# Optimization experiments

Measured on AMD Instinct MI355X. Metric: run time of the kernel, lower is better.

Reference implementation:

```python
import jax, jax.numpy as jnp
import numpy as np

MEAN, STD = 0.1307, 0.3081  # standard MNIST Normalization layer
FC = [784, 2048, 2048, 2048, 2048, 10]


def _forward_boxes(W, b, low, high):
    # swap bounds where weights are negative (interval arithmetic)
    Wn = jnp.where(W < 0, W, 0.0)
    Wp = jnp.where(W >= 0, W, 0.0)
    low_out = high @ Wn.T + low @ Wp.T + b
    high_out = low @ Wn.T + high @ Wp.T + b
    return low_out, high_out


def _abstract_relu(x, low, high):
    # vectorized DeepPoly relaxation (original loops per neuron)
    crossing = (low < 0) & (high > 0)
    denom = jnp.where(crossing, high - low, 1.0)  # safe denom
    ub_slope = jnp.where(crossing, high / denom, 0.0)
    ub_int = jnp.where(crossing, -(low * high) / denom, 0.0)
    lam = jnp.where(low * low > high * high, 0.0, 1.0)  # minimum-area lambda
    keep = jnp.where(high <= 0.0, 0.0, 1.0)  # identity diag unless dead neuron
    w_high = jnp.where(crossing, ub_slope, keep)
    w_low = jnp.where(crossing, lam, keep)
    b_high = ub_int
    x_out = jnp.maximum(x, 0.0)
    return x_out, w_low * low, w_high * high + b_high, (w_low, w_high, b_high)


def _back_sub_relu(M, w_high, w_low, b_high, is_high):
    # vectorized version of the original double python loop; w_* are the
    # relu diagonals ([in]), M is the accumulated backsub matrix [out,in]
    mask = (w_high != 0.0).astype(M.dtype)
    if is_high:
        out = jnp.where(M > 0, M * w_high, M * w_low) * mask
        bias = (jnp.maximum(M, 0.0) * mask) @ b_high
    else:
        out = jnp.where(M > 0, M * w_low, M * w_high) * mask
        bias = (jnp.minimum(M, 0.0) * mask) @ b_high
    return out, bias


def _back_sub(records, low0, high0, out_size):
    dt = low0.dtype
    Wl = jnp.eye(out_size, dtype=dt)
    Wh = jnp.eye(out_size, dtype=dt)
    bl = jnp.zeros(out_size, dtype=dt)
    bh = jnp.zeros(out_size, dtype=dt)
    for kind, data in reversed(records):
        if kind == 'linear':
            W, b = data
            bh = bh + Wh @ b
            bl = bl + Wl @ b
            Wh = Wh @ W
            Wl = Wl @ W
        else:  # relu
            wl, wh, bhr = data
            Wh, dbh = _back_sub_relu(Wh, wh, wl, bhr, True)
            Wl, dbl = _back_sub_relu(Wl, wh, wl, bhr, False)
            bh = bh + dbh
            bl = bl + dbl
    low_out, _ = _forward_boxes(Wl, bl, low0, high0)
    _, high_out = _forward_boxes(Wh, bh, low0, high0)
    return low_out, high_out


def _forward(x, low, high, params):
    norm = lambda t: ((t - MEAN) / STD).reshape(-1)
    x, low, high = norm(x), norm(low), norm(high)
    low0, high0 = low, high
    records = []
    n = len(params)
    for i, (W, b) in enumerate(params):
        x = W @ x + b
        records.append(('linear', (W, b)))
        # box bounds from forward_boxes are immediately replaced by backsub
        low, high = _back_sub(records, low0, high0, W.shape[0])
        if i + 1 < n:
            x, low, high, rdata = _abstract_relu(x, low, high)
            records.append(('relu', rdata))
    return x, low, high


def setup_inputs() -> dict:
    key = jax.random.key(0)
    ks = jax.random.split(key, 11)
    x = jax.random.normal(ks[0], (1, 1, 28, 28), dtype=jnp.float32)
    eps = 0.05
    inp = {"x": x, "low": x - eps, "high": x + eps}
    for i in range(5):
        fi, fo = FC[i], FC[i + 1]
        inp[f"W{i+1}"] = jax.random.normal(ks[1 + 2 * i], (fo, fi), dtype=jnp.float32) * float(1.0 / np.sqrt(fi))
        inp[f"b{i+1}"] = jax.random.normal(ks[2 + 2 * i], (fo,), dtype=jnp.float32) * 0.01
    return inp


def reference(x, low, high, W1, b1, W2, b2, W3, b3, W4, b4, W5, b5):
    params = [(W1, b1), (W2, b2), (W3, b3), (W4, b4), (W5, b5)]
    return _forward(x, low, high, params)
```

## Files before the change

### kernel.cpp

```cpp
#include <hip/hip_runtime.h>
#include <hip/hip_bf16.h>


#define MEAN_C 0.1307f
#define STD_C  0.3081f

#define OFF_X0     0u
#define OFF_X1     2048u
#define OFF_L0     4096u
#define OFF_H0     5120u
#define OFF_WL     6144u
#define OFF_WH     14336u
#define OFF_BHR    22528u
#define OFF_BOXA   30720u
#define OFF_BOXB   34816u
#define OFF_BIASA  38912u
#define OFF_BIASB  43008u
#define OFF_B20    47104u
#define OFF_W0TH   47136u
#define OFF_W0TL   964640u
#define OFF_W1TH   1882144u
#define OFF_W1TL   3979296u
#define OFF_W2TH   6076448u
#define OFF_W2TL   8173600u
#define OFF_AH0    10270752u
#define OFF_AL0    14465056u
#define OFF_AH1    18659360u
#define OFF_AL1    22853664u
#define OFF_PPA    18659360u
#define OFF_PPB    18987040u
#define OFF_PPC    19314720u
#define OFF_PPD    19642400u

typedef _Float16 half8 __attribute__((ext_vector_type(8)));
typedef float floatx4 __attribute__((ext_vector_type(4)));

__device__ __forceinline__ void gl2lds16(const void* g, void* l) {
    __builtin_amdgcn_global_load_lds(
        (const __attribute__((address_space(1))) unsigned int*)g,
        (__attribute__((address_space(3))) unsigned int*)l, 16, 0, 0);
}

__device__ __forceinline__ float blockReduce256(float v) {
    #pragma unroll
    for (int o = 32; o > 0; o >>= 1) v += __shfl_down(v, o, 64);
    __shared__ float sred[4];
    int w = threadIdx.x >> 6;
    if ((threadIdx.x & 63) == 0) sred[w] = v;
    __syncthreads();
    float r = 0.f;
    if (threadIdx.x == 0) r = sred[0] + sred[1] + sred[2] + sred[3];
    return r;
}

__device__ __forceinline__ float2 blockReduce256x2(float a, float b) {
    #pragma unroll
    for (int o = 32; o > 0; o >>= 1) {
        a += __shfl_down(a, o, 64);
        b += __shfl_down(b, o, 64);
    }
    __shared__ float sa[4], sb[4];
    int w = threadIdx.x >> 6;
    if ((threadIdx.x & 63) == 0) { sa[w] = a; sb[w] = b; }
    __syncthreads();
    float2 r = {0.f, 0.f};
    if (threadIdx.x == 0) {
        r.x = sa[0] + sa[1] + sa[2] + sa[3];
        r.y = sb[0] + sb[1] + sb[2] + sb[3];
    }
    return r;
}

__device__ __forceinline__ void relu_rec_calc(float h, float l,
                                              float& vwl, float& vwh, float& vbh) {
    if (h <= 0.f)      { vwl = 0.f; vwh = 0.f; vbh = 0.f; }
    else if (l >= 0.f) { vwl = 1.f; vwh = 1.f; vbh = 0.f; }
    else {
        float d = h - l;
        vwh = h / d;
        vbh = -(l * h) / d;
        vwl = (l * l > h * h) ? 0.f : 1.f;
    }
}

__global__ void k_norm(const float* __restrict__ x, const float* __restrict__ lo,
                       const float* __restrict__ hi, float* __restrict__ ws) {
    int i = blockIdx.x * blockDim.x + threadIdx.x;
    if (i < 784) {
        ws[OFF_X0 + i] = (x[i]  - MEAN_C) / STD_C;
        ws[OFF_L0 + i] = (lo[i] - MEAN_C) / STD_C;
        ws[OFF_H0 + i] = (hi[i] - MEAN_C) / STD_C;
    } else if (i < 896) {
        ws[OFF_L0 + i] = 0.f;
        ws[OFF_H0 + i] = 0.f;
    }
}

__global__ void k_fboxes0(const float* __restrict__ W0, const float* __restrict__ b0,
                          const float* __restrict__ x0,
                          const float* __restrict__ lo0, const float* __restrict__ hi0,
                          float* __restrict__ box, float* __restrict__ xout) {
    int r = blockIdx.x;
    int srow = r & 2047;
    int is_high = r < 2048;
    const float* Wr = W0 + (size_t)srow * 784;
    float acc = 0.f, accx = 0.f;
    for (int c = threadIdx.x; c < 784; c += 256) {
        float m = Wr[c];
        if (is_high) acc += (m < 0.f) ? m * lo0[c] : m * hi0[c];
        else         acc += (m < 0.f) ? m * hi0[c] : m * lo0[c];
        accx += m * x0[c];
    }
    float2 rr = blockReduce256x2(acc, accx);
    if (threadIdx.x == 0) {
        box[r] = rr.x + b0[srow];
        if (is_high) xout[r] = rr.y + b0[r];
    }
}

__global__ __launch_bounds__(256) void k_relu_split(
        const float* __restrict__ Wi, const float* __restrict__ xin,
        const float* __restrict__ boxPrev, const float* __restrict__ biasPrev,
        float* __restrict__ recWL, float* __restrict__ recWH, float* __restrict__ recBH,
        const float* __restrict__ bj, const float* __restrict__ bvi,
        float* __restrict__ bias, float* __restrict__ boxOut,
        float* __restrict__ xout,
        _Float16* __restrict__ Ahi, _Float16* __restrict__ Alo) {
    int row = blockIdx.x;
    int is_high = row < 2048;
    int srow = row & 2047;
    const float* src = Wi + (size_t)srow * 2048;
    int c0 = threadIdx.x * 8;
    float mv[8], bxh[8], bxl[8], abj[8], ax[8];
    *(float4*)&mv[0]  = *(const float4*)(src + c0);
    *(float4*)&mv[4]  = *(const float4*)(src + c0 + 4);
    *(float4*)&bxh[0] = *(const float4*)(boxPrev + c0);
    *(float4*)&bxh[4] = *(const float4*)(boxPrev + c0 + 4);
    *(float4*)&bxl[0] = *(const float4*)(boxPrev + 2048 + c0);
    *(float4*)&bxl[4] = *(const float4*)(boxPrev + 2048 + c0 + 4);
    *(float4*)&abj[0] = *(const float4*)(bj + c0);
    *(float4*)&abj[4] = *(const float4*)(bj + c0 + 4);
    *(float4*)&ax[0]  = *(const float4*)(xin + c0);
    *(float4*)&ax[4]  = *(const float4*)(xin + c0 + 4);
    if (biasPrev) {
        float ph[8], pl[8];
        *(float4*)&ph[0] = *(const float4*)(biasPrev + c0);
        *(float4*)&ph[4] = *(const float4*)(biasPrev + c0 + 4);
        *(float4*)&pl[0] = *(const float4*)(biasPrev + 2048 + c0);
        *(float4*)&pl[4] = *(const float4*)(biasPrev + 2048 + c0 + 4);
        #pragma unroll
        for (int e = 0; e < 8; e++) { bxh[e] += ph[e]; bxl[e] += pl[e]; }
    }
    float acc = 0.f, accx = 0.f;
    float rl[8], rh[8], rb[8];
    half8 hi, lo;
    #pragma unroll
    for (int e = 0; e < 8; e++) {
        relu_rec_calc(bxh[e], bxl[e], rl[e], rh[e], rb[e]);
        float m = mv[e];
        float t, bt;
        if (is_high) { t = (m > 0.f) ? m * rh[e] : m * rl[e]; bt = fmaxf(m, 0.f) * rb[e]; }
        else         { t = (m > 0.f) ? m * rl[e] : m * rh[e]; bt = fminf(m, 0.f) * rb[e]; }
        acc += bt + t * abj[e];
        accx += m * fmaxf(ax[e], 0.f);
        _Float16 h = (_Float16)t;
        hi[e] = h;
        lo[e] = (_Float16)(t - (float)h);
    }
    *(half8*)(Ahi + (size_t)row * 2048 + c0) = hi;
    *(half8*)(Alo + (size_t)row * 2048 + c0) = lo;
    if (row == 0) {
        *(float4*)(recWL + c0) = *(float4*)&rl[0];
        *(float4*)(recWL + c0 + 4) = *(float4*)&rl[4];
        *(float4*)(recWH + c0) = *(float4*)&rh[0];
        *(float4*)(recWH + c0 + 4) = *(float4*)&rh[4];
        *(float4*)(recBH + c0) = *(float4*)&rb[0];
        *(float4*)(recBH + c0 + 4) = *(float4*)&rb[4];
    }
    float2 rr = blockReduce256x2(acc, accx);
    if (threadIdx.x == 0) {
        bias[row] = bvi[srow] + rr.x;
        boxOut[row] = 0.f;
        if (is_high) xout[row] = rr.y + bvi[row];
    }
}

__global__ void k_transpose_split(const float* __restrict__ W, int NC,
                                  _Float16* __restrict__ Thi,
                                  _Float16* __restrict__ Tlo) {
    __shared__ float s[32][33];
    int c = threadIdx.x & 31;
    int r = threadIdx.x >> 5;
    #pragma unroll
    for (int rr = 0; rr < 4; rr++) {
        int k = blockIdx.y * 32 + r + rr * 8;
        int n = blockIdx.x * 32 + c;
        float v = (n < NC) ? W[(size_t)k * NC + n] : 0.f;
        s[c][r + rr * 8] = v;
    }
    __syncthreads();
    #pragma unroll
    for (int rr = 0; rr < 4; rr++) {
        int nl = r + rr * 8;
        float v = s[nl][c];
        _Float16 h = (_Float16)v;
        size_t o = (size_t)(blockIdx.x * 32 + nl) * 2048 + blockIdx.y * 32 + c;
        Thi[o] = h;
        Tlo[o] = (_Float16)(v - (float)h);
    }
}

template<int NT, int EPI>
__global__ __launch_bounds__(256, 2) void k_gemm(
        const _Float16* __restrict__ Ah, const _Float16* __restrict__ Al,
        const _Float16* __restrict__ Bh, const _Float16* __restrict__ Bl,
        const float* __restrict__ wl, const float* __restrict__ wh,
        const float* __restrict__ bhr, const float* __restrict__ bj,
        float* __restrict__ bias,
        _Float16* __restrict__ oAh, _Float16* __restrict__ oAl,
        const float* __restrict__ lo0, const float* __restrict__ hi0,
        float* __restrict__ box) {
    __shared__ _Float16 sAh[128 * 32], sAl[128 * 32];
    __shared__ _Float16 sBh[NT * 32 * 32], sBl[NT * 32 * 32];
    int tid = threadIdx.x;
    int row0 = blockIdx.y * 128, col0 = blockIdx.x * (NT * 32);

    int cr = tid >> 2;
    int q  = (tid & 3) ^ (cr & 3);
    const _Float16* gAh0 = Ah + (size_t)(row0 + cr) * 2048 + q * 8;
    const _Float16* gAh1 = gAh0 + (size_t)64 * 2048;
    const _Float16* gAl0 = Al + (size_t)(row0 + cr) * 2048 + q * 8;
    const _Float16* gAl1 = gAl0 + (size_t)64 * 2048;
    const _Float16* gBh0 = Bh + (size_t)(col0 + cr) * 2048 + q * 8;
    const _Float16* gBl0 = Bl + (size_t)(col0 + cr) * 2048 + q * 8;
    const _Float16* gBh1 = gBh0 + (size_t)64 * 2048;
    const _Float16* gBl1 = gBl0 + (size_t)64 * 2048;
    _Float16* lAh0 = &sAh[tid * 8];
    _Float16* lAh1 = &sAh[tid * 8 + 2048];
    _Float16* lAl0 = &sAl[tid * 8];
    _Float16* lAl1 = &sAl[tid * 8 + 2048];
    _Float16* lBh0 = &sBh[tid * 8];
    _Float16* lBl0 = &sBl[tid * 8];
    _Float16* lBh1 = &sBh[tid * 8 + 2048];
    _Float16* lBl1 = &sBl[tid * 8 + 2048];

    int lane = tid & 63, wv = tid >> 6;
    int wm = wv & 1, wn = wv >> 1;
    int l15 = lane & 15, lq = lane >> 4;
    int soff = (lq ^ (l15 & 3)) * 8;
    int arow = wm * 64 + l15;
    int brow = wn * (NT * 16) + l15;

    floatx4 acc[4][NT];
    floatx4 z = {0.f, 0.f, 0.f, 0.f};
    #pragma unroll
    for (int i = 0; i < 4; i++)
        #pragma unroll
        for (int j = 0; j < NT; j++) acc[i][j] = z;

    for (int k0 = 0; k0 < 2048; k0 += 32) {
        gl2lds16(gAh0 + k0, lAh0);
        gl2lds16(gAh1 + k0, lAh1);
        gl2lds16(gAl0 + k0, lAl0);
        gl2lds16(gAl1 + k0, lAl1);
        gl2lds16(gBh0 + k0, lBh0);
        gl2lds16(gBl0 + k0, lBl0);
        if (NT == 4) {
            gl2lds16(gBh1 + k0, lBh1);
            gl2lds16(gBl1 + k0, lBl1);
        }
        __syncthreads();
        half8 bh[NT], bl[NT];
        #pragma unroll
        for (int nt = 0; nt < NT; nt++) {
            bh[nt] = *(const half8*)&sBh[(brow + nt * 16) * 32 + soff];
            bl[nt] = *(const half8*)&sBl[(brow + nt * 16) * 32 + soff];
        }
        #pragma unroll
        for (int mt = 0; mt < 4; mt++) {
            half8 ah = *(const half8*)&sAh[(arow + mt * 16) * 32 + soff];
            half8 al = *(const half8*)&sAl[(arow + mt * 16) * 32 + soff];
            #pragma unroll
            for (int nt = 0; nt < NT; nt++) {
                acc[mt][nt] = __builtin_amdgcn_mfma_f32_16x16x32_f16(ah, bh[nt], acc[mt][nt], 0, 0, 0);
                acc[mt][nt] = __builtin_amdgcn_mfma_f32_16x16x32_f16(al, bh[nt], acc[mt][nt], 0, 0, 0);
                acc[mt][nt] = __builtin_amdgcn_mfma_f32_16x16x32_f16(ah, bl[nt], acc[mt][nt], 0, 0, 0);
            }
        }
        __syncthreads();
    }

    int is_high = row0 < 2048;
    float bsum[4][4];
    #pragma unroll
    for (int mt = 0; mt < 4; mt++)
        #pragma unroll
        for (int r = 0; r < 4; r++) bsum[mt][r] = 0.f;

    #pragma unroll
    for (int nt = 0; nt < NT; nt++) {
        int gc = col0 + wn * (NT * 16) + nt * 16 + l15;
        if (EPI == 0) {
            float cwl = wl[gc], cwh = wh[gc], cbh = bhr[gc], cbj = bj[gc];
            #pragma unroll
            for (int mt = 0; mt < 4; mt++) {
                #pragma unroll
                for (int r = 0; r < 4; r++) {
                    float m = acc[mt][nt][r];
                    float t, bt;
                    if (is_high) { t = (m > 0.f) ? m * cwh : m * cwl; bt = fmaxf(m, 0.f) * cbh; }
                    else         { t = (m > 0.f) ? m * cwl : m * cwh; bt = fminf(m, 0.f) * cbh; }
                    bsum[mt][r] += bt + t * cbj;
                    int grow = row0 + wm * 64 + mt * 16 + lq * 4 + r;
                    size_t o = (size_t)grow * 2048 + gc;
                    _Float16 h = (_Float16)t;
                    oAh[o] = h;
                    oAl[o] = (_Float16)(t - (float)h);
                }
            }
        } else {
            float clo = lo0[gc], chi = hi0[gc];
            #pragma unroll
            for (int mt = 0; mt < 4; mt++) {
                #pragma unroll
                for (int r = 0; r < 4; r++) {
                    float m = acc[mt][nt][r];
                    float contrib;
                    if (is_high) contrib = (m < 0.f) ? m * clo : m * chi;
                    else         contrib = (m < 0.f) ? m * chi : m * clo;
                    bsum[mt][r] += contrib;
                }
            }
        }
    }
    #pragma unroll
    for (int mt = 0; mt < 4; mt++) {
        #pragma unroll
        for (int r = 0; r < 4; r++) {
            float v = bsum[mt][r];
            v += __shfl_xor(v, 1);
            v += __shfl_xor(v, 2);
            v += __shfl_xor(v, 4);
            v += __shfl_xor(v, 8);
            if (l15 == 0) {
                int grow = row0 + wm * 64 + mt * 16 + lq * 4 + r;
                if (EPI == 0) atomicAdd(&bias[grow], v);
                else          atomicAdd(&box[grow], v);
            }
        }
    }
}

__global__ void k_relu_rec(const float* __restrict__ box, const float* __restrict__ bias,
                           float* __restrict__ wl, float* __restrict__ wh,
                           float* __restrict__ bhr) {
    int i = blockIdx.x * blockDim.x + threadIdx.x;
    float h = box[i] + bias[i];
    float l = box[2048 + i] + bias[2048 + i];
    float vwl, vwh, vbh;
    relu_rec_calc(h, l, vwl, vwh, vbh);
    wl[i] = vwl; wh[i] = vwh; bhr[i] = vbh;
}

__global__ __launch_bounds__(256) void k_skinny2(
        const float* __restrict__ src, int bcast,
        const float* __restrict__ wl, const float* __restrict__ wh,
        const float* __restrict__ W, int N, float* __restrict__ Ppart) {
    __shared__ float sA[20 * 256];
    __shared__ float sRed[20 * 128];
    int ky = blockIdx.y, k0 = ky * 256;
    int tid = threadIdx.x;
    for (int idx = tid; idx < 20 * 256; idx += 256) {
        int r = idx >> 8, c = idx & 255;
        int gc = k0 + c;
        float m;
        if (bcast) m = src[(size_t)(r % 10) * 2048 + gc];
        else {
            m = 0.f;
            #pragma unroll
            for (int p = 0; p < 8; p++)
                m += src[(size_t)p * 40960 + (size_t)r * 2048 + gc];
        }
        float t = (r < 10) ? ((m > 0.f) ? m * wh[gc] : m * wl[gc])
                           : ((m > 0.f) ? m * wl[gc] : m * wh[gc]);
        sA[idx] = t;
    }
    __syncthreads();
    int c = blockIdx.x * 128 + (tid & 127);
    int kh = tid >> 7;
    float acc[20];
    #pragma unroll
    for (int r = 0; r < 20; r++) acc[r] = 0.f;
    if (c < N) {
        const float* Wp = W + (size_t)(k0 + kh * 128) * N + c;
        for (int kk = 0; kk < 128; kk++) {
            float w = Wp[(size_t)kk * N];
            #pragma unroll
            for (int r = 0; r < 20; r++) acc[r] += sA[r * 256 + kh * 128 + kk] * w;
        }
    }
    if (kh == 1 && c < N) {
        #pragma unroll
        for (int r = 0; r < 20; r++) sRed[r * 128 + (tid & 127)] = acc[r];
    }
    __syncthreads();
    if (kh == 0 && c < N) {
        #pragma unroll
        for (int r = 0; r < 20; r++)
            Ppart[(size_t)ky * 40960 + (size_t)r * 2048 + c] =
                acc[r] + sRed[r * 128 + (tid & 127)];
    }
}

__global__ void k_bias20(const float* __restrict__ W4,
                         const float* __restrict__ PPa, const float* __restrict__ PPb,
                         const float* __restrict__ PPc,
                         const float* __restrict__ WLr, const float* __restrict__ WHr,
                         const float* __restrict__ BHr,
                         const float* __restrict__ b0, const float* __restrict__ b1,
                         const float* __restrict__ b2, const float* __restrict__ b3,
                         const float* __restrict__ b4,
                         const float* __restrict__ x3,
                         float* __restrict__ bias20, float* __restrict__ out) {
    int row = blockIdx.x;
    int is_high = row < 10;
    int srow = row % 10;
    float acc = 0.f, accx = 0.f;
    for (int c = threadIdx.x; c < 2048; c += 256) {
        {
            float m = W4[(size_t)srow * 2048 + c];
            float wlv = WLr[3 * 2048 + c], whv = WHr[3 * 2048 + c], bhv = BHr[3 * 2048 + c];
            float t  = is_high ? ((m > 0.f) ? m * whv : m * wlv) : ((m > 0.f) ? m * wlv : m * whv);
            float bt = is_high ? fmaxf(m, 0.f) * bhv : fminf(m, 0.f) * bhv;
            acc += bt + t * b3[c];
            accx += m * fmaxf(x3[c], 0.f);
        }
        {
            float m = 0.f;
            #pragma unroll
            for (int p = 0; p < 8; p++) m += PPa[(size_t)p * 40960 + (size_t)row * 2048 + c];
            float wlv = WLr[2 * 2048 + c], whv = WHr[2 * 2048 + c], bhv = BHr[2 * 2048 + c];
            float t  = is_high ? ((m > 0.f) ? m * whv : m * wlv) : ((m > 0.f) ? m * wlv : m * whv);
            float bt = is_high ? fmaxf(m, 0.f) * bhv : fminf(m, 0.f) * bhv;
            acc += bt + t * b2[c];
        }
        {
            float m = 0.f;
            #pragma unroll
            for (int p = 0; p < 8; p++) m += PPb[(size_t)p * 40960 + (size_t)row * 2048 + c];
            float wlv = WLr[1 * 2048 + c], whv = WHr[1 * 2048 + c], bhv = BHr[1 * 2048 + c];
            float t  = is_high ? ((m > 0.f) ? m * whv : m * wlv) : ((m > 0.f) ? m * wlv : m * whv);
            float bt = is_high ? fmaxf(m, 0.f) * bhv : fminf(m, 0.f) * bhv;
            acc += bt + t * b1[c];
        }
        {
            float m = 0.f;
            #pragma unroll
            for (int p = 0; p < 8; p++) m += PPc[(size_t)p * 40960 + (size_t)row * 2048 + c];
            float wlv = WLr[c], whv = WHr[c], bhv = BHr[c];
            float t  = is_high ? ((m > 0.f) ? m * whv : m * wlv) : ((m > 0.f) ? m * wlv : m * whv);
            float bt = is_high ? fmaxf(m, 0.f) * bhv : fminf(m, 0.f) * bhv;
            acc += bt + t * b0[c];
        }
    }
    float2 rr = blockReduce256x2(acc, accx);
    if (threadIdx.x == 0) {
        bias20[row] = b4[srow] + rr.x;
        if (is_high) out[row] = b4[row] + rr.y;
    }
}

__global__ void k_fbox20(const float* __restrict__ Ppart,
                         const float* __restrict__ bias20,
                         const float* __restrict__ lo0, const float* __restrict__ hi0,
                         float* __restrict__ out) {
    int row = blockIdx.x;
    int is_high = row < 10;
    float acc = 0.f;
    for (int c = threadIdx.x; c < 784; c += 256) {
        float m = 0.f;
        #pragma unroll
        for (int p = 0; p < 8; p++)
            m += Ppart[(size_t)p * 40960 + (size_t)row * 2048 + c];
        if (is_high) acc += (m < 0.f) ? m * lo0[c] : m * hi0[c];
        else         acc += (m < 0.f) ? m * hi0[c] : m * lo0[c];
    }
    acc = blockReduce256(acc);
    if (threadIdx.x == 0) {
        float v = acc + bias20[row];
        out[is_high ? (20 + row) : row] = v;
    }
}

extern "C" void kernel_launch(void* const* d_in, const int* in_sizes, int n_in,
                              void* d_out, int out_size, void* d_ws, size_t ws_size,
                              hipStream_t stream) {
    const float* x_in  = (const float*)d_in[0];
    const float* lo_in = (const float*)d_in[1];
    const float* hi_in = (const float*)d_in[2];
    const float* W[5];
    const float* bv[5];
    for (int i = 0; i < 5; i++) {
        W[i]  = (const float*)d_in[3 + 2 * i];
        bv[i] = (const float*)d_in[4 + 2 * i];
    }
    float* ws = (float*)d_ws;
    float* out = (float*)d_out;

    float* X[2]    = {ws + OFF_X0, ws + OFF_X1};
    float* lo0     = ws + OFF_L0;
    float* hi0     = ws + OFF_H0;
    float* BOX[2]  = {ws + OFF_BOXA, ws + OFF_BOXB};
    float* BIAS[2] = {ws + OFF_BIASA, ws + OFF_BIASB};
    float* b20     = ws + OFF_B20;
    float* PPa     = ws + OFF_PPA;
    float* PPb     = ws + OFF_PPB;
    float* PPc     = ws + OFF_PPC;
    float* PPd     = ws + OFF_PPD;
    _Float16* WT_H[3] = {(_Float16*)(ws + OFF_W0TH), (_Float16*)(ws + OFF_W1TH),
                         (_Float16*)(ws + OFF_W2TH)};
    _Float16* WT_L[3] = {(_Float16*)(ws + OFF_W0TL), (_Float16*)(ws + OFF_W1TL),
                         (_Float16*)(ws + OFF_W2TL)};
    _Float16* AH[2] = {(_Float16*)(ws + OFF_AH0), (_Float16*)(ws + OFF_AH1)};
    _Float16* AL[2] = {(_Float16*)(ws + OFF_AL0), (_Float16*)(ws + OFF_AL1)};
    float* WLr = ws + OFF_WL;
    float* WHr = ws + OFF_WH;
    float* BHr = ws + OFF_BHR;

    k_norm<<<4, 256, 0, stream>>>(x_in, lo_in, hi_in, ws);
    k_transpose_split<<<dim3(28, 64), 256, 0, stream>>>(W[0], 784, WT_H[0], WT_L[0]);
    k_transpose_split<<<dim3(64, 64), 256, 0, stream>>>(W[1], 2048, WT_H[1], WT_L[1]);
    k_transpose_split<<<dim3(64, 64), 256, 0, stream>>>(W[2], 2048, WT_H[2], WT_L[2]);

    k_fboxes0<<<4096, 256, 0, stream>>>(W[0], bv[0], X[0], lo0, hi0, BOX[0], X[1]);

    int xcur = 1, bprev = 0;
    const float* biasPrev = nullptr;
    for (int i = 1; i <= 3; i++) {
        int xnxt = xcur ^ 1;
        int bcur = bprev ^ 1;
        float* biasCur = BIAS[(i - 1) & 1];
        k_relu_split<<<4096, 256, 0, stream>>>(
            W[i], X[xcur], BOX[bprev], biasPrev,
            WLr + (i - 1) * 2048, WHr + (i - 1) * 2048, BHr + (i - 1) * 2048,
            bv[i - 1], bv[i], biasCur, BOX[bcur], X[xnxt], AH[0], AL[0]);
        int p = 0;
        for (int j = i - 1; j >= 1; j--) {
            k_gemm<4, 0><<<dim3(16, 32), 256, 0, stream>>>(
                AH[p], AL[p], WT_H[j], WT_L[j],
                WLr + (j - 1) * 2048, WHr + (j - 1) * 2048,
                BHr + (j - 1) * 2048, bv[j - 1], biasCur,
                AH[p ^ 1], AL[p ^ 1], nullptr, nullptr, nullptr);
            p ^= 1;
        }
        k_gemm<2, 1><<<dim3(14, 32), 256, 0, stream>>>(
            AH[p], AL[p], WT_H[0], WT_L[0],
            nullptr, nullptr, nullptr, nullptr, nullptr,
            nullptr, nullptr, lo0, hi0, BOX[bcur]);
        biasPrev = biasCur;
        bprev = bcur;
        xcur = xnxt;
    }
    k_relu_rec<<<8, 256, 0, stream>>>(BOX[bprev], BIAS[0],
                                      WLr + 3 * 2048, WHr + 3 * 2048, BHr + 3 * 2048);

    k_skinny2<<<dim3(16, 8), 256, 0, stream>>>(W[4], 1,
        WLr + 3 * 2048, WHr + 3 * 2048, W[3], 2048, PPa);
    k_skinny2<<<dim3(16, 8), 256, 0, stream>>>(PPa, 0,
        WLr + 2 * 2048, WHr + 2 * 2048, W[2], 2048, PPb);
    k_skinny2<<<dim3(16, 8), 256, 0, stream>>>(PPb, 0,
        WLr + 1 * 2048, WHr + 1 * 2048, W[1], 2048, PPc);
    k_skinny2<<<dim3(7, 8), 256, 0, stream>>>(PPc, 0,
        WLr, WHr, W[0], 784, PPd);
    k_bias20<<<20, 256, 0, stream>>>(W[4], PPa, PPb, PPc,
        WLr, WHr, BHr, bv[0], bv[1], bv[2], bv[3], bv[4], X[xcur], b20, out);
    k_fbox20<<<20, 256, 0, stream>>>(PPd, b20, lo0, hi0, out);
}
```

Measured before the change: 891.1 us.

## Double-buffer LDS tiles in split-fp16 GEMM to overlap loads with MFMA

Converts the k-loop of the split-precision GEMM into a two-stage LDS ping-pong pipeline. Global-to-LDS copies for tile t+2 are issued right after the fragments of tile t are read into registers, with vmcnt waits and explicit barriers replacing the two __syncthreads per iteration. The aim is to hide global memory latency behind MFMA work. In exchange it doubles shared memory use, which may cut occupancy under launch_bounds(256,2), and the hand-counted waitcnts are fragile.

```diff
diff --git a/kernel.cpp b/kernel.cpp
--- a/kernel.cpp
+++ b/kernel.cpp
@@ -220,8 +220,8 @@
         _Float16* __restrict__ oAh, _Float16* __restrict__ oAl,
         const float* __restrict__ lo0, const float* __restrict__ hi0,
         float* __restrict__ box) {
-    __shared__ _Float16 sAh[128 * 32], sAl[128 * 32];
-    __shared__ _Float16 sBh[NT * 32 * 32], sBl[NT * 32 * 32];
+    __shared__ _Float16 sAh[2][128 * 32], sAl[2][128 * 32];
+    __shared__ _Float16 sBh[2][NT * 32 * 32], sBl[2][NT * 32 * 32];
     int tid = threadIdx.x;
     int row0 = blockIdx.y * 128, col0 = blockIdx.x * (NT * 32);
 
@@ -235,14 +235,7 @@
     const _Float16* gBl0 = Bl + (size_t)(col0 + cr) * 2048 + q * 8;
     const _Float16* gBh1 = gBh0 + (size_t)64 * 2048;
     const _Float16* gBl1 = gBl0 + (size_t)64 * 2048;
-    _Float16* lAh0 = &sAh[tid * 8];
-    _Float16* lAh1 = &sAh[tid * 8 + 2048];
-    _Float16* lAl0 = &sAl[tid * 8];
-    _Float16* lAl1 = &sAl[tid * 8 + 2048];
-    _Float16* lBh0 = &sBh[tid * 8];
-    _Float16* lBl0 = &sBl[tid * 8];
-    _Float16* lBh1 = &sBh[tid * 8 + 2048];
-    _Float16* lBl1 = &sBl[tid * 8 + 2048];
+    int loff = tid * 8;
 
     int lane = tid & 63, wv = tid >> 6;
     int wm = wv & 1, wn = wv >> 1;
@@ -258,36 +251,63 @@
         #pragma unroll
         for (int j = 0; j < NT; j++) acc[i][j] = z;
 
-    for (int k0 = 0; k0 < 2048; k0 += 32) {
-        gl2lds16(gAh0 + k0, lAh0);
-        gl2lds16(gAh1 + k0, lAh1);
-        gl2lds16(gAl0 + k0, lAl0);
-        gl2lds16(gAl1 + k0, lAl1);
-        gl2lds16(gBh0 + k0, lBh0);
-        gl2lds16(gBl0 + k0, lBl0);
+    auto STAGE = [&](int b, int k0) {
+        gl2lds16(gAh0 + k0, &sAh[b][loff]);
+        gl2lds16(gAh1 + k0, &sAh[b][loff + 2048]);
+        gl2lds16(gAl0 + k0, &sAl[b][loff]);
+        gl2lds16(gAl1 + k0, &sAl[b][loff + 2048]);
+        gl2lds16(gBh0 + k0, &sBh[b][loff]);
+        gl2lds16(gBl0 + k0, &sBl[b][loff]);
         if (NT == 4) {
-            gl2lds16(gBh1 + k0, lBh1);
-            gl2lds16(gBl1 + k0, lBl1);
-        }
-        __syncthreads();
-        half8 bh[NT], bl[NT];
+            gl2lds16(gBh1 + k0, &sBh[b][loff + 2048]);
+            gl2lds16(gBl1 + k0, &sBl[b][loff + 2048]);
+        }
+    };
+
+    STAGE(0, 0);
+    STAGE(1, 32);
+    if constexpr (NT == 4) asm volatile("s_waitcnt vmcnt(8)" ::: "memory");
+    else                   asm volatile("s_waitcnt vmcnt(6)" ::: "memory");
+    __builtin_amdgcn_s_barrier();
+    __builtin_amdgcn_sched_barrier(0);
+
+    for (int t = 0; t < 64; ++t) {
+        int cur = t & 1;
+        half8 bh[NT], bl[NT], ah4[4], al4[4];
         #pragma unroll
         for (int nt = 0; nt < NT; nt++) {
-            bh[nt] = *(const half8*)&sBh[(brow + nt * 16) * 32 + soff];
-            bl[nt] = *(const half8*)&sBl[(brow + nt * 16) * 32 + soff];
+            bh[nt] = *(const half8*)&sBh[cur][(brow + nt * 16) * 32 + soff];
+            bl[nt] = *(const half8*)&sBl[cur][(brow + nt * 16) * 32 + soff];
         }
         #pragma unroll
         for (int mt = 0; mt < 4; mt++) {
-            half8 ah = *(const half8*)&sAh[(arow + mt * 16) * 32 + soff];
-            half8 al = *(const half8*)&sAl[(arow + mt * 16) * 32 + soff];
+            ah4[mt] = *(const half8*)&sAh[cur][(arow + mt * 16) * 32 + soff];
+            al4[mt] = *(const half8*)&sAl[cur][(arow + mt * 16) * 32 + soff];
+        }
+        asm volatile("s_waitcnt lgkmcnt(0)" ::: "memory");
+        __builtin_amdgcn_sched_barrier(0);
+        __builtin_amdgcn_s_barrier();
+        __builtin_amdgcn_sched_barrier(0);
+        if (t < 62) STAGE(cur, (t + 2) * 32);
+        #pragma unroll
+        for (int mt = 0; mt < 4; mt++) {
             #pragma unroll
             for (int nt = 0; nt < NT; nt++) {
-                acc[mt][nt] = __builtin_amdgcn_mfma_f32_16x16x32_f16(ah, bh[nt], acc[mt][nt], 0, 0, 0);
-                acc[mt][nt] = __builtin_amdgcn_mfma_f32_16x16x32_f16(al, bh[nt], acc[mt][nt], 0, 0, 0);
-                acc[mt][nt] = __builtin_amdgcn_mfma_f32_16x16x32_f16(ah, bl[nt], acc[mt][nt], 0, 0, 0);
+                acc[mt][nt] = __builtin_amdgcn_mfma_f32_16x16x32_f16(ah4[mt], bh[nt], acc[mt][nt], 0, 0, 0);
+                acc[mt][nt] = __builtin_amdgcn_mfma_f32_16x16x32_f16(al4[mt], bh[nt], acc[mt][nt], 0, 0, 0);
+                acc[mt][nt] = __builtin_amdgcn_mfma_f32_16x16x32_f16(ah4[mt], bl[nt], acc[mt][nt], 0, 0, 0);
             }
         }
-        __syncthreads();
+        if (t < 63) {
+            if (t < 62) {
+                if constexpr (NT == 4) asm volatile("s_waitcnt vmcnt(8)" ::: "memory");
+                else                   asm volatile("s_waitcnt vmcnt(6)" ::: "memory");
+            } else {
+                asm volatile("s_waitcnt vmcnt(0)" ::: "memory");
+            }
+            __builtin_amdgcn_s_barrier();
+            __builtin_amdgcn_sched_barrier(0);
+        }
     }
 
     int is_high = row0 < 2048;
```

Result: faster. 867.5 us (-2.6%).
